# Optimization experiments

Measured on AMD Instinct MI355X. Metric: run time of the kernel, lower is better.

## Reference

```python
import jax, jax.numpy as jnp
import numpy as np
from jax import lax

NH = 8          # num_heads
DK = 256        # depth_k
DV = 256        # depth_v
DKH = DK // NH  # per-head key depth
DVH = DV // NH  # per-head value depth


def setup_inputs() -> dict:
    key = jax.random.key(0)
    k1, k2, k3 = jax.random.split(key, 3)
    B, C, H, W = 8, 256, 32, 32
    x = jax.random.normal(k1, (B, C, H, W), dtype=jnp.float32)
    # fan-in scaled init (glorot-like) to keep conv outputs / attention logits sane
    conv_w = jax.random.normal(k2, (3, 3, 256, 256), dtype=jnp.float32) / np.sqrt(3 * 3 * 256)
    conv_b = jnp.zeros((256,), dtype=jnp.float32)
    attn_w = jax.random.normal(k3, (1, 1, 256, 768), dtype=jnp.float32) / np.sqrt(256)
    attn_b = jnp.zeros((768,), dtype=jnp.float32)
    return {"x": x, "conv_w": conv_w, "conv_b": conv_b, "attn_w": attn_w, "attn_b": attn_b}


def _conv2d_same(x, w, b):
    # x: (B,C,H,W), w: (kh,kw,Cin,Cout) -> (B,Cout,H,W)
    y = lax.conv_general_dilated(x, w, window_strides=(1, 1), padding="SAME",
                                 dimension_numbers=("NCHW", "HWIO", "NCHW"))
    return y + b[None, :, None, None]


def reference(x, conv_w, conv_b, attn_w, attn_b):
    B, C, H, W = x.shape
    HW = H * W

    # parallel conv branch: channels_out - depth_v = 256 output channels
    conv_out = _conv2d_same(x, conv_w, conv_b)

    # 1x1 conv producing K, Q, V (split order matches tf.split([dk, dk, dv]))
    kqv = _conv2d_same(x, attn_w, attn_b)
    k = kqv[:, :DK]
    q = kqv[:, DK:2 * DK] * (DKH ** -0.5)
    v = kqv[:, 2 * DK:]

    # (B, Nh, d, HW) per-head flattening; token axis = HW
    def heads(t, d):
        return t.reshape(B, NH, d, HW)

    qh, kh, vh = heads(q, DKH), heads(k, DKH), heads(v, DVH)

    # logits: (B, Nh, HW, HW)
    logits = jnp.einsum("bhdn,bhdm->bhnm", qh, kh)
    weights = jax.nn.softmax(logits, axis=-1)
    # attn: (B, Nh, HW, dvh)
    attn = jnp.einsum("bhnm,bhdm->bhnd", weights, vh)

    # combine heads: (B,Nh,H,W,dvh) -> channel order (nh, dvh) -> (B, depth_v, H, W)
    attn_out = attn.reshape(B, NH, H, W, DVH).transpose(0, 1, 4, 2, 3).reshape(B, DV, H, W)

    return jnp.concatenate([conv_out, attn_out], axis=1)
```

## Files before the change

### kernel.cpp

```cpp
#include <hip/hip_runtime.h>


typedef __attribute__((ext_vector_type(8))) short short8;
typedef __attribute__((ext_vector_type(4))) float f32x4;
typedef __attribute__((ext_vector_type(16))) float f32x16;
typedef unsigned short u16;

#define QSCALE 0.25503487629898483f

__device__ inline u16 f2bf(float f) {
  unsigned u = __builtin_bit_cast(unsigned, f);
  return (u16)((u + 0x7FFFu + ((u >> 16) & 1u)) >> 16);
}
__device__ inline unsigned pack2bf(float a, float b) {
  return (unsigned)f2bf(a) | ((unsigned)f2bf(b) << 16);
}
__device__ inline unsigned packP(float a, float b) {
  unsigned au = __builtin_bit_cast(unsigned, a) + 0x8000u;
  unsigned bu = __builtin_bit_cast(unsigned, b) + 0x8000u;
  return __builtin_amdgcn_perm(bu, au, 0x07060302u);
}

__global__ __launch_bounds__(256) void prep_kernel(const float* __restrict__ x,
                                                   const float* __restrict__ cw,
                                                   const float* __restrict__ aw,
                                                   u16* __restrict__ xT,
                                                   u16* __restrict__ WcT,
                                                   u16* __restrict__ WaT) {
  __shared__ float T[64][65];
  int bid = blockIdx.x, tid = threadIdx.x;

  if (bid < 128) {
    int b = bid >> 4, n0 = (bid & 15) * 64;
#pragma unroll
    for (int rep = 0; rep < 2; ++rep) {
      int flat = rep * 256 + tid;
      int n = flat & 63, cg = flat >> 6;
#pragma unroll
      for (int q = 0; q < 4; ++q) {
        short8 pk;
#pragma unroll
        for (int j = 0; j < 8; ++j)
          pk[j] =
              (short)f2bf(x[(b * 256 + cg * 32 + q * 8 + j) * 1024 + n0 + n]);
        *(short8*)&xT[(b * 1024 + n0 + n) * 256 + cg * 32 + q * 8] = pk;
      }
    }
    return;
  }

  int tt = bid - 128;
  int chunk = tt >> 4, t = tt & 15;
  int ci0 = (t & 3) * 64, r0 = (t >> 2) * 64;
  bool isconv = chunk < 9;
  float scale = (chunk == 10) ? QSCALE : 1.0f;

#pragma unroll
  for (int rep = 0; rep < 16; ++rep) {
    int flat = rep * 256 + tid;
    int i = flat >> 6, j = flat & 63;
    T[i][j] = isconv ? cw[(chunk * 256 + ci0 + i) * 256 + r0 + j]
                     : aw[(ci0 + i) * 768 + (chunk - 9) * 256 + r0 + j];
  }
  __syncthreads();
#pragma unroll
  for (int rep = 0; rep < 4; ++rep) {
    int flat = rep * 256 + tid;
    int jj = flat >> 4, qq = flat & 15;
    float v0 = T[qq * 4 + 0][jj] * scale;
    float v1 = T[qq * 4 + 1][jj] * scale;
    float v2 = T[qq * 4 + 2][jj] * scale;
    float v3 = T[qq * 4 + 3][jj] * scale;
    uint2 pk = {pack2bf(v0, v1), pack2bf(v2, v3)};
    if (isconv)
      *(uint2*)&WcT[(chunk * 256 + r0 + jj) * 256 + ci0 + qq * 4] = pk;
    else
      *(uint2*)&WaT[((chunk - 9) * 256 + r0 + jj) * 256 + ci0 + qq * 4] = pk;
  }
}

__global__ __launch_bounds__(256) void kqv_kernel(const u16* __restrict__ xT,
                                                  const u16* __restrict__ WaT,
                                                  const float* __restrict__ ab,
                                                  u16* __restrict__ kT,
                                                  u16* __restrict__ qT,
                                                  u16* __restrict__ vB) {
  __shared__ __align__(16) u16 Tt[64 * 136];
  int bid = blockIdx.x;
  int b = bid & 7, idx = bid >> 3;
  int ot = idx >> 4, nt = idx & 15;
  int tid = threadIdx.x, wave = tid >> 6, lane = tid & 63;
  int ln = lane & 15, g = lane >> 4;
  int o0 = ot * 128 + (wave & 1) * 64;
  int n0 = nt * 64 + (wave >> 1) * 32;
  const u16* xb = xT + b * 1024 * 256;
  f32x4 acc[4][2];
#pragma unroll
  for (int i = 0; i < 4; ++i)
#pragma unroll
    for (int j = 0; j < 2; ++j) acc[i][j] = (f32x4){0.f, 0.f, 0.f, 0.f};

#pragma unroll
  for (int c0 = 0; c0 < 256; c0 += 32) {
    int ko = c0 + g * 8;
    short8 a0 = *(const short8*)&WaT[(o0 + ln) * 256 + ko];
    short8 a1 = *(const short8*)&WaT[(o0 + 16 + ln) * 256 + ko];
    short8 a2 = *(const short8*)&WaT[(o0 + 32 + ln) * 256 + ko];
    short8 a3 = *(const short8*)&WaT[(o0 + 48 + ln) * 256 + ko];
    short8 b0 = *(const short8*)&xb[(n0 + ln) * 256 + ko];
    short8 b1 = *(const short8*)&xb[(n0 + 16 + ln) * 256 + ko];
    acc[0][0] = __builtin_amdgcn_mfma_f32_16x16x32_bf16(a0, b0, acc[0][0], 0, 0, 0);
    acc[0][1] = __builtin_amdgcn_mfma_f32_16x16x32_bf16(a0, b1, acc[0][1], 0, 0, 0);
    acc[1][0] = __builtin_amdgcn_mfma_f32_16x16x32_bf16(a1, b0, acc[1][0], 0, 0, 0);
    acc[1][1] = __builtin_amdgcn_mfma_f32_16x16x32_bf16(a1, b1, acc[1][1], 0, 0, 0);
    acc[2][0] = __builtin_amdgcn_mfma_f32_16x16x32_bf16(a2, b0, acc[2][0], 0, 0, 0);
    acc[2][1] = __builtin_amdgcn_mfma_f32_16x16x32_bf16(a2, b1, acc[2][1], 0, 0, 0);
    acc[3][0] = __builtin_amdgcn_mfma_f32_16x16x32_bf16(a3, b0, acc[3][0], 0, 0, 0);
    acc[3][1] = __builtin_amdgcn_mfma_f32_16x16x32_bf16(a3, b1, acc[3][1], 0, 0, 0);
  }

  if (ot >= 4) {
#pragma unroll
    for (int it = 0; it < 4; ++it)
#pragma unroll
      for (int r = 0; r < 4; ++r) {
        int o = o0 + it * 16 + g * 4 + r;
        float bias = ab[o];
#pragma unroll
        for (int jt = 0; jt < 2; ++jt) {
          int n = n0 + jt * 16 + ln;
          vB[(b * 256 + (o - 512)) * 1024 + n] = f2bf(acc[it][jt][r] + bias);
        }
      }
    return;
  }

  bool isQ = (ot >= 2);
  float bs = isQ ? QSCALE : 1.0f;
  int olb = (wave & 1) * 64;
  int nlb = (wave >> 1) * 32;
#pragma unroll
  for (int it = 0; it < 4; ++it)
#pragma unroll
    for (int jt = 0; jt < 2; ++jt) {
      int ol = olb + it * 16 + g * 4;
      int nl = nlb + jt * 16 + ln;
      int og = ot * 128 + ol;
      float v0 = acc[it][jt][0] + ab[og + 0] * bs;
      float v1 = acc[it][jt][1] + ab[og + 1] * bs;
      float v2 = acc[it][jt][2] + ab[og + 2] * bs;
      float v3 = acc[it][jt][3] + ab[og + 3] * bs;
      uint2 pk = {pack2bf(v0, v1), pack2bf(v2, v3)};
      *(uint2*)&Tt[nl * 136 + ol] = pk;
    }
  __syncthreads();
  u16* dst = isQ ? qT : kT;
#pragma unroll
  for (int rep = 0; rep < 4; ++rep) {
    int flat = rep * 256 + tid;
    int o8 = flat & 15, nl = flat >> 4;
    short8 v = *(const short8*)&Tt[nl * 136 + o8 * 8];
    int og256 = (ot & 1) * 128 + o8 * 8;
    int hh = og256 >> 5, d0 = og256 & 31;
    int ng = nt * 64 + nl;
    *(short8*)&dst[((b * 8 + hh) * 1024 + ng) * 32 + d0] = v;
  }
}

__global__ __launch_bounds__(256, 2) void conv_attn_kernel(
    const u16* __restrict__ xT, const u16* __restrict__ WcT,
    const float* __restrict__ cb, const u16* __restrict__ kT,
    const u16* __restrict__ qT, const u16* __restrict__ vB,
    float* __restrict__ out) {
  __shared__ __align__(16) unsigned char smem[19584];

  int bid = blockIdx.x;
  int b = bid & 7;
  int sub = bid >> 3;
  int trip = sub / 3;
  int rem = sub - trip * 3;
  int tid = threadIdx.x;
  int wave = tid >> 6, lane = tid & 63;

  if (rem == 2) {
    int ln = lane & 15, g = lane >> 4;
    u16* Xc = (u16*)smem;
    int hp = trip >> 1, coh = trip & 1;
    int h0 = hp * 2;
    int co0 = coh * 128 + wave * 32;

    f32x4 acc[2][4];
#pragma unroll
    for (int i = 0; i < 2; ++i)
#pragma unroll
      for (int j = 0; j < 4; ++j) acc[i][j] = (f32x4){0.f, 0.f, 0.f, 0.f};

    {
      int rp = tid >> 6, rest = tid & 63;
      int which = rest >> 5, cp = rest & 31;
      *(unsigned*)&Xc[(rp * 34 + which * 33) * 72 + cp * 2] = 0u;
    }

    for (int c0 = 0; c0 < 256; c0 += 64) {
      __syncthreads();
#pragma unroll
      for (int rep = 0; rep < 4; ++rep) {
        int flat = rep * 256 + tid;
        int cg = flat & 7, w = (flat >> 3) & 31, rp = flat >> 8;
        int row = h0 - 1 + rp;
        short8 v = {0, 0, 0, 0, 0, 0, 0, 0};
        if ((unsigned)row < 32u)
          v = *(const short8*)&xT[(b * 1024 + row * 32 + w) * 256 + c0 + cg * 8];
        int rowS = rp * 34 + w + 1;
        *(short8*)&Xc[rowS * 72 + ((cg ^ (rowS & 7)) * 8)] = v;
      }
      __syncthreads();
#pragma unroll
      for (int ks = 0; ks < 2; ++ks) {
        int ko = c0 + ks * 32 + g * 8;
        int slot = ks * 4 + g;
#pragma unroll
        for (int r = 0; r < 3; ++r)
#pragma unroll
          for (int s = 0; s < 3; ++s) {
            int tap = r * 3 + s;
            short8 a0 = *(const short8*)&WcT[(tap * 256 + co0 + ln) * 256 + ko];
            short8 a1 =
                *(const short8*)&WcT[(tap * 256 + co0 + 16 + ln) * 256 + ko];
#pragma unroll
            for (int jt = 0; jt < 4; ++jt) {
              int rowp = ((jt >> 1) + r) * 34 + (jt & 1) * 16 + ln + s;
              short8 bf =
                  *(const short8*)&Xc[rowp * 72 + ((slot ^ (rowp & 7)) * 8)];
              acc[0][jt] = __builtin_amdgcn_mfma_f32_16x16x32_bf16(
                  a0, bf, acc[0][jt], 0, 0, 0);
              acc[1][jt] = __builtin_amdgcn_mfma_f32_16x16x32_bf16(
                  a1, bf, acc[1][jt], 0, 0, 0);
            }
          }
      }
    }

#pragma unroll
    for (int it = 0; it < 2; ++it)
#pragma unroll
      for (int r4 = 0; r4 < 4; ++r4) {
        int co = co0 + it * 16 + g * 4 + r4;
        float bias = cb[co];
#pragma unroll
        for (int jt = 0; jt < 4; ++jt) {
          int h = h0 + (jt >> 1), w = (jt & 1) * 16 + ln;
          out[((b * 512 + co) * 32 + h) * 32 + w] = acc[it][jt][r4] + bias;
        }
      }
    return;
  }

  u16* kvb = (u16*)smem;
  int idx = trip * 2 + rem;
  int h = idx >> 3, qt = idx & 7;
  int nw = qt * 128 + wave * 32;
  int lq = lane & 31, hi = lane >> 5;

  const u16* kb = kT + (b * 8 + h) * (1024 * 32);
  const u16* qb = qT + (b * 8 + h) * (1024 * 32);
  const u16* vb = vB + (b * 256 + h * 32) * 1024;

  short8 qf0 = *(const short8*)&qb[(nw + lq) * 32 + hi * 8];
  short8 qf1 = *(const short8*)&qb[(nw + lq) * 32 + 16 + hi * 8];

  int sr = tid >> 2, ss = tid & 3;
  int dvr = tid >> 3, vs = tid & 7;
  const u16* ksrc = kb + sr * 32 + ss * 8;
  const u16* vsrc = vb + dvr * 1024 + vs * 8;
  int kdst = sr * 40 + ss * 8;
  int vdst = 2560 + dvr * 72 + vs * 8;

  int kr0 = lq * 40;
  int kr1 = (32 + lq) * 40;
  int vr = 2560 + lq * 72;

  f32x16 o0 = {};
  float mx = -1e30f, l = 0.f;

  short8 kp = *(const short8*)ksrc;
  short8 vp = *(const short8*)vsrc;
  *(short8*)&kvb[kdst] = kp;
  *(short8*)&kvb[vdst] = vp;
  __syncthreads();
  kp = *(const short8*)(ksrc + 2048);
  vp = *(const short8*)(vsrc + 64);

  for (int mt = 0; mt < 16; ++mt) {
    u16* bc = kvb + (mt & 1) * 4864;
    if (mt < 15) {
      u16* bn = kvb + ((mt + 1) & 1) * 4864;
      *(short8*)&bn[kdst] = kp;
      *(short8*)&bn[vdst] = vp;
    }
    if (mt < 14) {
      kp = *(const short8*)(ksrc + (mt + 2) * 2048);
      vp = *(const short8*)(vsrc + (mt + 2) * 64);
    }

    short8 ka00 = *(const short8*)&bc[kr0 + hi * 8];
    short8 ka01 = *(const short8*)&bc[kr0 + 16 + hi * 8];
    short8 ka10 = *(const short8*)&bc[kr1 + hi * 8];
    short8 ka11 = *(const short8*)&bc[kr1 + 16 + hi * 8];
    f32x16 s0t = {}, s1t = {};
    __builtin_amdgcn_s_setprio(1);
    s0t = __builtin_amdgcn_mfma_f32_32x32x16_bf16(ka00, qf0, s0t, 0, 0, 0);
    s0t = __builtin_amdgcn_mfma_f32_32x32x16_bf16(ka01, qf1, s0t, 0, 0, 0);
    s1t = __builtin_amdgcn_mfma_f32_32x32x16_bf16(ka10, qf0, s1t, 0, 0, 0);
    s1t = __builtin_amdgcn_mfma_f32_32x32x16_bf16(ka11, qf1, s1t, 0, 0, 0);
    __builtin_amdgcn_s_setprio(0);

    short8 vf0 = *(const short8*)&bc[vr + hi * 8];
    short8 vf1 = *(const short8*)&bc[vr + 16 + hi * 8];
    short8 vf2 = *(const short8*)&bc[vr + 32 + hi * 8];
    short8 vf3 = *(const short8*)&bc[vr + 48 + hi * 8];

    float tmax = s0t[0];
#pragma unroll
    for (int r = 1; r < 16; ++r) tmax = fmaxf(tmax, s0t[r]);
#pragma unroll
    for (int r = 0; r < 16; ++r) tmax = fmaxf(tmax, s1t[r]);
    tmax = fmaxf(tmax, __shfl_xor(tmax, 32));

    if (!__all(tmax - mx <= 8.0f)) {
      float nm = fmaxf(mx, tmax);
      float sc = __builtin_amdgcn_exp2f(mx - nm);
#pragma unroll
      for (int r = 0; r < 16; ++r) o0[r] *= sc;
      l *= sc;
      mx = nm;
    }

#pragma unroll
    for (int r = 0; r < 16; ++r) {
      s0t[r] = __builtin_amdgcn_exp2f(s0t[r] - mx);
      s1t[r] = __builtin_amdgcn_exp2f(s1t[r] - mx);
    }
    float ts = 0.f;
#pragma unroll
    for (int r = 0; r < 16; ++r) ts += s0t[r] + s1t[r];
    ts += __shfl_xor(ts, 32);
    l += ts;

    __builtin_amdgcn_s_setprio(1);
#define PV_CHUNK(SV, CB, VF)                                                  \
  {                                                                           \
    unsigned A0 = packP(SV[(CB) + 0], SV[(CB) + 1]);                          \
    unsigned A1 = packP(SV[(CB) + 2], SV[(CB) + 3]);                          \
    unsigned B0 = packP(SV[(CB) + 4], SV[(CB) + 5]);                          \
    unsigned B1 = packP(SV[(CB) + 6], SV[(CB) + 7]);                          \
    unsigned sm0 = hi ? A0 : B0, sm1 = hi ? A1 : B1;                          \
    unsigned r0_ = (unsigned)__shfl_xor((int)sm0, 32);                        \
    unsigned r1_ = (unsigned)__shfl_xor((int)sm1, 32);                        \
    uint4 fw;                                                                 \
    fw.x = hi ? r0_ : A0;                                                     \
    fw.y = hi ? r1_ : A1;                                                     \
    fw.z = hi ? B0 : r0_;                                                     \
    fw.w = hi ? B1 : r1_;                                                     \
    short8 pf = __builtin_bit_cast(short8, fw);                               \
    o0 = __builtin_amdgcn_mfma_f32_32x32x16_bf16(VF, pf, o0, 0, 0, 0);        \
  }
    PV_CHUNK(s0t, 0, vf0)
    PV_CHUNK(s0t, 8, vf1)
    PV_CHUNK(s1t, 0, vf2)
    PV_CHUNK(s1t, 8, vf3)
#undef PV_CHUNK
    __builtin_amdgcn_s_setprio(0);

    __syncthreads();
  }

  float rl = 1.f / l;
  float* ob = out + (b * 512 + 256 + h * 32) * 1024 + nw + lq;
#pragma unroll
  for (int r = 0; r < 16; ++r) {
    int dv = (r & 3) + 8 * (r >> 2) + 4 * hi;
    ob[dv * 1024] = o0[r] * rl;
  }
}

extern "C" void kernel_launch(void* const* d_in, const int* in_sizes, int n_in,
                              void* d_out, int out_size, void* d_ws,
                              size_t ws_size, hipStream_t stream) {
  const float* x  = (const float*)d_in[0];
  const float* cw = (const float*)d_in[1];
  const float* cb = (const float*)d_in[2];
  const float* aw = (const float*)d_in[3];
  const float* ab = (const float*)d_in[4];
  float* out = (float*)d_out;

  char* ws = (char*)d_ws;
  u16* vB  = (u16*)ws;
  u16* kT  = (u16*)(ws + 4194304);
  u16* qT  = (u16*)(ws + 8388608);
  u16* xT  = (u16*)(ws + 12582912);
  u16* WcT = (u16*)(ws + 16777216);
  u16* WaT = (u16*)(ws + 17956864);

  prep_kernel<<<320, 256, 0, stream>>>(x, cw, aw, xT, WcT, WaT);
  kqv_kernel<<<768, 256, 0, stream>>>(xT, WaT, ab, kT, qT, vB);
  conv_attn_kernel<<<768, 256, 0, stream>>>(xT, WcT, cb, kT, qT, vB, out);
}
```

Measured before the change: 65.39 us.

## Stage kqv GEMM operands through double-buffered LDS and use cheaper bf16 packing

The kqv projection kernel now cooperatively loads the weight and activation tiles into a padded, double-buffered shared-memory buffer, with register prefetch of the next K-slice. Each wave then reads its MFMA fragments from LDS instead of issuing redundant global loads. This removes duplicated global traffic across waves at the cost of a barrier per K-step. The prep kernel also swaps per-element bf16 rounding for the perm-based packP, which rounds half away from zero instead of to even.

```diff
diff --git a/kernel.cpp b/kernel.cpp
--- a/kernel.cpp
+++ b/kernel.cpp
@@ -36,14 +36,17 @@
     for (int rep = 0; rep < 2; ++rep) {
       int flat = rep * 256 + tid;
       int n = flat & 63, cg = flat >> 6;
+      const float* xs = x + b * 256 * 1024 + n0 + n;
 #pragma unroll
       for (int q = 0; q < 4; ++q) {
-        short8 pk;
-#pragma unroll
-        for (int j = 0; j < 8; ++j)
-          pk[j] =
-              (short)f2bf(x[(b * 256 + cg * 32 + q * 8 + j) * 1024 + n0 + n]);
-        *(short8*)&xT[(b * 1024 + n0 + n) * 256 + cg * 32 + q * 8] = pk;
+        uint4 pk;
+#pragma unroll
+        for (int jj = 0; jj < 4; ++jj) {
+          float a = xs[(cg * 32 + q * 8 + 2 * jj) * 1024];
+          float c = xs[(cg * 32 + q * 8 + 2 * jj + 1) * 1024];
+          ((unsigned*)&pk)[jj] = packP(a, c);
+        }
+        *(uint4*)&xT[(b * 1024 + n0 + n) * 256 + cg * 32 + q * 8] = pk;
       }
     }
     return;
@@ -85,7 +88,7 @@
                                                   u16* __restrict__ kT,
                                                   u16* __restrict__ qT,
                                                   u16* __restrict__ vB) {
-  __shared__ __align__(16) u16 Tt[64 * 136];
+  __shared__ __align__(16) u16 S[15360];
   int bid = blockIdx.x;
   int b = bid & 7, idx = bid >> 3;
   int ot = idx >> 4, nt = idx & 15;
@@ -94,21 +97,41 @@
   int o0 = ot * 128 + (wave & 1) * 64;
   int n0 = nt * 64 + (wave >> 1) * 32;
   const u16* xb = xT + b * 1024 * 256;
+
+  int rA = tid >> 2, slA = tid & 3;
+  const u16* aS0 = WaT + (ot * 128 + rA) * 256 + slA * 8;
+  const u16* aS1 = aS0 + 64 * 256;
+  const u16* bS = xb + (nt * 64 + rA) * 256 + slA * 8;
+  int aD0 = rA * 40 + slA * 8;
+  int aD1 = aD0 + 64 * 40;
+  int bD = 5120 + rA * 40 + slA * 8;
+
+  int aF = ((wave & 1) * 64 + ln) * 40 + g * 8;
+  int bF = 5120 + ((wave >> 1) * 32 + ln) * 40 + g * 8;
+
   f32x4 acc[4][2];
 #pragma unroll
   for (int i = 0; i < 4; ++i)
 #pragma unroll
     for (int j = 0; j < 2; ++j) acc[i][j] = (f32x4){0.f, 0.f, 0.f, 0.f};
 
-#pragma unroll
-  for (int c0 = 0; c0 < 256; c0 += 32) {
-    int ko = c0 + g * 8;
-    short8 a0 = *(const short8*)&WaT[(o0 + ln) * 256 + ko];
-    short8 a1 = *(const short8*)&WaT[(o0 + 16 + ln) * 256 + ko];
-    short8 a2 = *(const short8*)&WaT[(o0 + 32 + ln) * 256 + ko];
-    short8 a3 = *(const short8*)&WaT[(o0 + 48 + ln) * 256 + ko];
-    short8 b0 = *(const short8*)&xb[(n0 + ln) * 256 + ko];
-    short8 b1 = *(const short8*)&xb[(n0 + 16 + ln) * 256 + ko];
+  *(short8*)&S[aD0] = *(const short8*)aS0;
+  *(short8*)&S[aD1] = *(const short8*)aS1;
+  *(short8*)&S[bD] = *(const short8*)bS;
+  __syncthreads();
+  short8 pa0 = *(const short8*)(aS0 + 32);
+  short8 pa1 = *(const short8*)(aS1 + 32);
+  short8 pb = *(const short8*)(bS + 32);
+
+#pragma unroll
+  for (int s = 0; s < 8; ++s) {
+    const u16* buf = S + (s & 1) * 7680;
+    short8 a0 = *(const short8*)&buf[aF];
+    short8 a1 = *(const short8*)&buf[aF + 16 * 40];
+    short8 a2 = *(const short8*)&buf[aF + 32 * 40];
+    short8 a3 = *(const short8*)&buf[aF + 48 * 40];
+    short8 b0 = *(const short8*)&buf[bF];
+    short8 b1 = *(const short8*)&buf[bF + 16 * 40];
     acc[0][0] = __builtin_amdgcn_mfma_f32_16x16x32_bf16(a0, b0, acc[0][0], 0, 0, 0);
     acc[0][1] = __builtin_amdgcn_mfma_f32_16x16x32_bf16(a0, b1, acc[0][1], 0, 0, 0);
     acc[1][0] = __builtin_amdgcn_mfma_f32_16x16x32_bf16(a1, b0, acc[1][0], 0, 0, 0);
@@ -117,6 +140,18 @@
     acc[2][1] = __builtin_amdgcn_mfma_f32_16x16x32_bf16(a2, b1, acc[2][1], 0, 0, 0);
     acc[3][0] = __builtin_amdgcn_mfma_f32_16x16x32_bf16(a3, b0, acc[3][0], 0, 0, 0);
     acc[3][1] = __builtin_amdgcn_mfma_f32_16x16x32_bf16(a3, b1, acc[3][1], 0, 0, 0);
+    if (s < 7) {
+      u16* nb = S + ((s + 1) & 1) * 7680;
+      *(short8*)&nb[aD0] = pa0;
+      *(short8*)&nb[aD1] = pa1;
+      *(short8*)&nb[bD] = pb;
+      if (s < 6) {
+        pa0 = *(const short8*)(aS0 + (s + 2) * 32);
+        pa1 = *(const short8*)(aS1 + (s + 2) * 32);
+        pb = *(const short8*)(bS + (s + 2) * 32);
+      }
+    }
+    __syncthreads();
   }
 
   if (ot >= 4) {
@@ -135,6 +170,7 @@
     return;
   }
 
+  u16* Tt = S;
   bool isQ = (ot >= 2);
   float bs = isQ ? QSCALE : 1.0f;
   int olb = (wave & 1) * 64;
```

After: 54.71 us. -16.3%, faster.
